# Performance work log

Hardware: AMD Instinct MI355X
Metric: run time of the kernel (lower is better)

The kernel has to match this reference:

```python
import math
import jax, jax.numpy as jnp
import numpy as np

B, N, T, C, H = 16, 307, 24, 128, 8
D = C // H
FACTOR = 5
S = min(FACTOR * int(np.ceil(np.log(T))), T)   # sample_k (U_part) = 20
U = S                                          # n_top u = 20


def _pos_emb(t_len, c):
    pos = jnp.arange(t_len, dtype=jnp.float32)[:, None]
    div = jnp.exp(jnp.arange(0, c, 2, dtype=jnp.float32) * (-math.log(10000.0) / c))
    pe = jnp.zeros((t_len, c), dtype=jnp.float32)
    pe = pe.at[:, 0::2].set(jnp.sin(pos * div))
    pe = pe.at[:, 1::2].set(jnp.cos(pos * div))
    return pe  # [T, C]


def _layernorm(x, g, b, eps=1e-5):
    m = x.mean(-1, keepdims=True)
    v = ((x - m) ** 2).mean(-1, keepdims=True)
    return (x - m) / jnp.sqrt(v + eps) * g + b


def _forward(query, time_encoder, index_sample,
             emb_minute, emb_hour, emb_weekday, emb_month, emb_year,
             Wq, Wk, Wv, Wo, bo, ff_w1, ff_b1, ff_w2, ff_b2,
             ln1_g, ln1_b, ln2_g, ln2_b):
    # DataEmbedding: x + positional + temporal (dropout = identity in eval)
    pe = _pos_emb(T, C)                                   # [T, C]
    te = (emb_minute[time_encoder[..., 0]] + emb_hour[time_encoder[..., 1]]
          + emb_weekday[time_encoder[..., 2]] + emb_month[time_encoder[..., 3]]
          + emb_year[time_encoder[..., 4]])               # [B, T, C]
    x = query + pe[None, None, :, :] + te[:, None, :, :]  # [B, N, T, C]

    # QKV projections -> [B, H, N, T, D]
    def proj(inp, W):
        return (inp @ W).reshape(B, N, T, H, D).transpose(0, 3, 1, 2, 4)
    Q, K, V = proj(x, Wq), proj(x, Wk), proj(x, Wv)

    # ProbSparse: sample S keys per query position
    K_samp = K[:, :, :, index_sample, :]                  # [B, H, N, T, S, D]
    QK_samp = jnp.einsum('bhntd,bhntsd->bhnts', Q, K_samp)
    M = QK_samp.max(-1) - QK_samp.sum(-1) / S             # [B, H, N, T]
    _, M_top = jax.lax.top_k(M, U)                        # [B, H, N, U]

    Q_red = jnp.take_along_axis(Q, M_top[..., None], axis=3)  # [B, H, N, U, D]
    scores = jnp.einsum('bhnud,bhntd->bhnut', Q_red, K) * (1.0 / math.sqrt(D))
    attn = jax.nn.softmax(scores, axis=-1)
    upd = jnp.einsum('bhnut,bhntd->bhnud', attn, V)       # [B, H, N, U, D]

    # initial context = mean over T, then scatter-update top-u query rows
    ctx = jnp.broadcast_to(V.mean(axis=3, keepdims=True), V.shape)
    ctx = ctx.at[jnp.arange(B)[:, None, None, None],
                 jnp.arange(H)[None, :, None, None],
                 jnp.arange(N)[None, None, :, None],
                 M_top].set(upd)

    ctx = ctx.transpose(0, 2, 3, 1, 4).reshape(B, N, T, C)
    att_out = ctx @ Wo + bo

    x1 = _layernorm(att_out + x, ln1_g, ln1_b)
    ff = jax.nn.relu(x1 @ ff_w1 + ff_b1) @ ff_w2 + ff_b2
    out = _layernorm(ff + x1, ln2_g, ln2_b)
    return out


def setup_inputs() -> dict:
    key = jax.random.key(0)
    ks = jax.random.split(key, 32)
    def nrm(i, shape, s=0.02):
        return jax.random.normal(ks[i], shape, dtype=jnp.float32) * s
    inp = {
        'value': jax.random.normal(ks[0], (B, N, T, C), dtype=jnp.float32),
        'key_in': jax.random.normal(ks[1], (B, N, T, C), dtype=jnp.float32),
        'query': jax.random.normal(ks[2], (B, N, T, C), dtype=jnp.float32),
        't': 1,
        'time_encoder': jax.random.randint(ks[3], (B, T, 5), 0, 10),
        'index_sample': jax.random.randint(ks[4], (T, S), 0, T),
        'emb_minute': nrm(5, (70, C), 1.0), 'emb_hour': nrm(6, (30, C), 1.0),
        'emb_weekday': nrm(7, (10, C), 1.0), 'emb_month': nrm(8, (40, C), 1.0),
        'emb_year': nrm(9, (400, C), 1.0),
        'Wq': nrm(10, (C, C)), 'Wk': nrm(11, (C, C)), 'Wv': nrm(12, (C, C)),
        'Wo': nrm(13, (C, C)), 'bo': jnp.zeros((C,), jnp.float32),
        'ff_w1': nrm(14, (C, 4 * C)), 'ff_b1': jnp.zeros((4 * C,), jnp.float32),
        'ff_w2': nrm(15, (4 * C, C)), 'ff_b2': jnp.zeros((C,), jnp.float32),
        'ln1_g': jnp.ones((C,), jnp.float32), 'ln1_b': jnp.zeros((C,), jnp.float32),
        'ln2_g': jnp.ones((C,), jnp.float32), 'ln2_b': jnp.zeros((C,), jnp.float32),
    }
    return inp


def reference(value, key_in, query, t, time_encoder, index_sample,
              emb_minute, emb_hour, emb_weekday, emb_month, emb_year,
              Wq, Wk, Wv, Wo, bo, ff_w1, ff_b1, ff_w2, ff_b2,
              ln1_g, ln1_b, ln2_g, ln2_b):
    # value, key_in, t are accepted but unused, matching the torch module
    return _forward(query, time_encoder, index_sample,
                    emb_minute, emb_hour, emb_weekday, emb_month, emb_year,
                    Wq, Wk, Wv, Wo, bo, ff_w1, ff_b1, ff_w2, ff_b2,
                    ln1_g, ln1_b, ln2_g, ln2_b)
```

## Files before the change

kernel.cpp:

```cpp
#include <hip/hip_runtime.h>
#include <hip/hip_bf16.h>
#include <cmath>

namespace {
constexpr int B_ = 16, N_ = 307, T_ = 24, C_ = 128, H_ = 8, D_ = 16, S_ = 20, U_ = 20;
constexpr int NROW = B_ * N_ * T_;
constexpr int NX = NROW * C_;
constexpr int TEPE_N = B_ * T_ * C_;
constexpr int FF = 4 * C_;
constexpr int BM = 32;
constexpr int NBLK_MM = NROW / BM;
constexpr int BMT = 32;
constexpr int NBLK_T = NROW / BMT;
constexpr int NUNIT = B_ * H_ * N_;
}

typedef __attribute__((ext_vector_type(8))) short short8;
typedef __attribute__((ext_vector_type(4))) short short4_;
typedef __attribute__((ext_vector_type(4))) float f32x4;

__device__ inline short f2bf(float v) {
    union { float f; unsigned u; } a; a.f = v;
    unsigned r = a.u + 0x7fff + ((a.u >> 16) & 1);
    return (short)(r >> 16);
}
__device__ inline float bf2f(short s) {
    return __bfloat162float(*(const __hip_bfloat16*)&s);
}

__global__ void k_tepe(const int* __restrict__ te,
                       const float* __restrict__ e_min, const float* __restrict__ e_hr,
                       const float* __restrict__ e_wd, const float* __restrict__ e_mo,
                       const float* __restrict__ e_yr, float* __restrict__ tepe,
                       const int* __restrict__ idxs, unsigned char* __restrict__ cntg) {
    int i = blockIdx.x * blockDim.x + threadIdx.x;
    if (i < TEPE_N) {
        int c = i & (C_ - 1);
        int bt = i >> 7;
        int t = bt % T_;
        const int* enc = te + bt * 5;
        float v = e_min[enc[0] * C_ + c] + e_hr[enc[1] * C_ + c] + e_wd[enc[2] * C_ + c]
                + e_mo[enc[3] * C_ + c] + e_yr[enc[4] * C_ + c];
        float ang = (float)t * expf(-(float)(c & ~1) * (9.210340371976184f / 128.0f));
        v += (c & 1) ? cosf(ang) : sinf(ang);
        tepe[i] = v;
    }
    if (blockIdx.x == 0) {
        __shared__ int scnt[T_ * 32];
        for (int j = threadIdx.x; j < T_ * 32; j += 256) scnt[j] = 0;
        __syncthreads();
        for (int j = threadIdx.x; j < T_ * S_; j += 256) {
            int t = j / S_;
            atomicAdd(&scnt[t * 32 + idxs[j]], 1);
        }
        __syncthreads();
        for (int j = threadIdx.x; j < 192; j += 256) {
            unsigned v = (unsigned)scnt[4 * j] | ((unsigned)scnt[4 * j + 1] << 8)
                       | ((unsigned)scnt[4 * j + 2] << 16) | ((unsigned)scnt[4 * j + 3] << 24);
            ((unsigned*)cntg)[j] = v;
        }
    }
}

__global__ void k_wcvt_qkv(const float* __restrict__ Wq, const float* __restrict__ Wk,
                           const float* __restrict__ Wv, short* __restrict__ wqkvf) {
    int i = blockIdx.x * 256 + threadIdx.x;
    int tile = i >> 9, l = (i >> 3) & 63, e = i & 7;
    int c_tile = tile >> 2, ks = tile & 3;
    int c_all = c_tile * 16 + (l & 15);
    int k = ks * 32 + (l >> 4) * 8 + e;
    int m = c_all >> 7, c = c_all & (C_ - 1);
    const float* W = (m == 0) ? Wq : (m == 1) ? Wk : Wv;
    wqkvf[i] = f2bf(W[k * C_ + c]);
}

__global__ void k_wcvt2(const float* __restrict__ w1, const float* __restrict__ w2,
                        const float* __restrict__ Wo,
                        short* __restrict__ w1f, short* __restrict__ w2f,
                        short* __restrict__ wof) {
    int i = blockIdx.x * 256 + threadIdx.x;
    if (i < C_ * FF) {
        int tile = i >> 9, l = (i >> 3) & 63, e = i & 7;
        int jtile = tile >> 2, ks = tile & 3;
        int j = jtile * 16 + (l & 15);
        int k = ks * 32 + (l >> 4) * 8 + e;
        w1f[i] = f2bf(w1[k * FF + j]);
    } else if (i < 2 * C_ * FF) {
        int i2 = i - C_ * FF;
        int tile = i2 >> 9, l = (i2 >> 3) & 63, e = i2 & 7;
        int c_tile = tile >> 4, ks = tile & 15;
        int c = c_tile * 16 + (l & 15);
        int j = ks * 32 + (l >> 4) * 8 + e;
        w2f[i2] = f2bf(w2[j * C_ + c]);
    } else {
        int i3 = i - 2 * C_ * FF;
        int tile = i3 >> 9, l = (i3 >> 3) & 63, e = i3 & 7;
        int c_tile = tile >> 2, ks = tile & 3;
        int c = c_tile * 16 + (l & 15);
        int k = ks * 32 + (l >> 4) * 8 + e;
        wof[i3] = f2bf(Wo[k * C_ + c]);
    }
}

__global__ __launch_bounds__(256) void k_qkv_mfma(
    const float* __restrict__ query, const float* __restrict__ tepe,
    const short* __restrict__ wqkvf,
    short* __restrict__ Q, short* __restrict__ K, short* __restrict__ V) {
    __shared__ __align__(16) short xs[BM * C_];
    int tid = threadIdx.x;
    int r0 = blockIdx.x * BM;
    {
        int row = tid >> 3;
        int cb = (tid & 7) * 16;
        int gr = r0 + row;
        int t = gr % T_;
        int b = gr / (N_ * T_);
        const float* qsrc = query + (size_t)gr * C_ + cb;
        const float* tsrc = tepe + (size_t)(b * T_ + t) * C_ + cb;
        int swz0 = (row & 7) << 3;
#pragma unroll
        for (int i = 0; i < 4; i++) {
            float4 q4 = *(const float4*)(qsrc + 4 * i);
            float4 t4 = *(const float4*)(tsrc + 4 * i);
            short4_ sv;
            sv.x = f2bf(q4.x + t4.x); sv.y = f2bf(q4.y + t4.y);
            sv.z = f2bf(q4.z + t4.z); sv.w = f2bf(q4.w + t4.w);
            *(short4_*)&xs[(row * C_ + cb + 4 * i) ^ swz0] = sv;
        }
    }
    __syncthreads();
    int w = tid >> 6, l = tid & 63;
    int lr = l & 15, lk = l >> 4;
    int swz = (lr & 7) << 3;
    short8 bx[2][4];
#pragma unroll
    for (int rt = 0; rt < 2; rt++)
#pragma unroll
        for (int ks = 0; ks < 4; ks++)
            bx[rt][ks] = *(const short8*)&xs[((rt * 16 + lr) * C_ + ks * 32 + lk * 8) ^ swz];
    size_t base[2];
#pragma unroll
    for (int rt = 0; rt < 2; rt++) {
        int gr = r0 + rt * 16 + lr;
        int t = gr % T_;
        int n = (gr / T_) % N_;
        int b = gr / (N_ * T_);
        base[rt] = ((size_t)b * H_ * N_ + n) * (T_ * D_) + t * D_;
    }
#pragma unroll
    for (int jt = 0; jt < 6; jt++) {
        int ctile = w * 6 + jt;
        const short* ap = wqkvf + (size_t)ctile * 2048 + l * 8;
        short8 acur[4];
#pragma unroll
        for (int ks = 0; ks < 4; ks++) acur[ks] = *(const short8*)(ap + ks * 512);
        f32x4 acc[2] = {{0.f, 0.f, 0.f, 0.f}, {0.f, 0.f, 0.f, 0.f}};
#pragma unroll
        for (int ks = 0; ks < 4; ks++) {
#pragma unroll
            for (int rt = 0; rt < 2; rt++)
                acc[rt] = __builtin_amdgcn_mfma_f32_16x16x32_bf16(acur[ks], bx[rt][ks], acc[rt], 0, 0, 0);
        }
        int c0 = ctile * 16 + lk * 4;
        int m = c0 >> 7;
        int c = c0 & (C_ - 1);
        int h = c >> 4, d = c & 15;
        short* dst = (m == 0) ? Q : (m == 1) ? K : V;
#pragma unroll
        for (int rt = 0; rt < 2; rt++) {
            short4_ sv;
            sv.x = f2bf(acc[rt][0]); sv.y = f2bf(acc[rt][1]);
            sv.z = f2bf(acc[rt][2]); sv.w = f2bf(acc[rt][3]);
            *(short4_*)&dst[base[rt] + (size_t)h * (N_ * T_ * D_) + d] = sv;
        }
    }
}

__global__ __launch_bounds__(256) void k_attn(
    const short* __restrict__ Q, const short* __restrict__ K, const short* __restrict__ V,
    const unsigned char* __restrict__ cntg, short* __restrict__ ctx) {
    __shared__ __align__(16) short Qbf[4][32 * 24], Kbf[4][32 * 24];
    __shared__ __align__(16) short Vt[4][16 * 40];
    __shared__ __align__(16) short Pbf[4][32 * 40];
    __shared__ unsigned char cntS[T_ * 32];
    __shared__ float Mv[4][T_];
    __shared__ int keepS[4][T_];
    __shared__ float meanVs[4][D_];
    int tid = threadIdx.x;
    int wid = tid >> 6, l = tid & 63;
    int e = blockIdx.x * 4 + wid;
    const short* qb = Q + (size_t)e * (T_ * D_);
    const short* kb = K + (size_t)e * (T_ * D_);
    const short* vb = V + (size_t)e * (T_ * D_);
    if (l < 48) {
        int t = l >> 1, hf = l & 1;
        *(short8*)&Qbf[wid][t * 24 + hf * 8] = *(const short8*)(qb + t * 16 + hf * 8);
        *(short8*)&Kbf[wid][t * 24 + hf * 8] = *(const short8*)(kb + t * 16 + hf * 8);
    }
    for (int i = l; i < 96; i += 64) {
        int t = i >> 2, c4 = i & 3;
        short4_ v = *(const short4_*)(vb + t * 16 + c4 * 4);
        Vt[wid][(c4 * 4 + 0) * 40 + t] = v.x;
        Vt[wid][(c4 * 4 + 1) * 40 + t] = v.y;
        Vt[wid][(c4 * 4 + 2) * 40 + t] = v.z;
        Vt[wid][(c4 * 4 + 3) * 40 + t] = v.w;
    }
    for (int i = l; i < 128; i += 64) {
        int d = i >> 3, c = 24 + (i & 7);
        Vt[wid][d * 40 + c] = 0;
    }
    if (tid < 192) ((int*)cntS)[tid] = ((const int*)cntg)[tid];
    __syncthreads();
    if (l >= 48) {
        int d = l - 48;
        float s = 0.f;
        for (int t = 0; t < T_; t++) s += bf2f(Vt[wid][d * 40 + t]);
        meanVs[wid][d] = s * (1.0f / T_);
    }
    int lr = l & 15, lk = l >> 4;
    short8 zz = {};
    short8 kf0 = zz, kf1 = zz, qf0 = zz, qf1 = zz;
    if (lk < 2) {
        kf0 = *(const short8*)&Kbf[wid][lr * 24 + lk * 8];
        kf1 = *(const short8*)&Kbf[wid][(16 + lr) * 24 + lk * 8];
        qf0 = *(const short8*)&Qbf[wid][lr * 24 + lk * 8];
        qf1 = *(const short8*)&Qbf[wid][(16 + lr) * 24 + lk * 8];
    }
    f32x4 zf = {0.f, 0.f, 0.f, 0.f};
    f32x4 s00 = __builtin_amdgcn_mfma_f32_16x16x32_bf16(kf0, qf0, zf, 0, 0, 0);
    f32x4 s01 = __builtin_amdgcn_mfma_f32_16x16x32_bf16(kf1, qf0, zf, 0, 0, 0);
    f32x4 s10 = __builtin_amdgcn_mfma_f32_16x16x32_bf16(kf0, qf1, zf, 0, 0, 0);
    f32x4 s11 = __builtin_amdgcn_mfma_f32_16x16x32_bf16(kf1, qf1, zf, 0, 0, 0);
#pragma unroll
    for (int rt = 0; rt < 2; rt++) {
        int t = rt * 16 + lr;
        int tt = (t < T_) ? t : 0;
        f32x4 c0 = rt ? s10 : s00;
        f32x4 c1 = rt ? s11 : s01;
        float mx = -1e30f, sm = 0.f;
#pragma unroll
        for (int i = 0; i < 4; i++) {
            int cA = cntS[tt * 32 + lk * 4 + i];
            if (cA) { mx = fmaxf(mx, c0[i]); sm += (float)cA * c0[i]; }
        }
        if (lk < 2) {
#pragma unroll
            for (int i = 0; i < 4; i++) {
                int cB = cntS[tt * 32 + 16 + lk * 4 + i];
                if (cB) { mx = fmaxf(mx, c1[i]); sm += (float)cB * c1[i]; }
            }
        }
        mx = fmaxf(mx, __shfl_xor(mx, 16));
        mx = fmaxf(mx, __shfl_xor(mx, 32));
        sm += __shfl_xor(sm, 16);
        sm += __shfl_xor(sm, 32);
        if (lk == 0 && t < T_) Mv[wid][t] = mx - sm * (1.0f / S_);
    }
    __syncthreads();
    if (l < T_) {
        float mt = Mv[wid][l];
        int cnt2 = 0;
        for (int t2 = 0; t2 < T_; t2++) {
            float m2 = Mv[wid][t2];
            cnt2 += (m2 > mt) || (m2 == mt && t2 < l);
        }
        keepS[wid][l] = (cnt2 < U_) ? 1 : 0;
    }
#pragma unroll
    for (int rt = 0; rt < 2; rt++) {
        f32x4 c0 = rt ? s10 : s00;
        f32x4 c1 = rt ? s11 : s01;
        float lm = fmaxf(fmaxf(c0[0], c0[1]), fmaxf(c0[2], c0[3]));
        if (lk < 2) lm = fmaxf(lm, fmaxf(fmaxf(c1[0], c1[1]), fmaxf(c1[2], c1[3])));
        lm = fmaxf(lm, __shfl_xor(lm, 16));
        lm = fmaxf(lm, __shfl_xor(lm, 32));
        float e0[4], e1[4];
        float ls = 0.f;
#pragma unroll
        for (int i = 0; i < 4; i++) { e0[i] = __expf(0.25f * (c0[i] - lm)); ls += e0[i]; }
#pragma unroll
        for (int i = 0; i < 4; i++) { e1[i] = (lk < 2) ? __expf(0.25f * (c1[i] - lm)) : 0.f; ls += e1[i]; }
        ls += __shfl_xor(ls, 16);
        ls += __shfl_xor(ls, 32);
        float inv = 1.0f / ls;
        short4_ w0, w1;
        w0.x = f2bf(e0[0] * inv); w0.y = f2bf(e0[1] * inv);
        w0.z = f2bf(e0[2] * inv); w0.w = f2bf(e0[3] * inv);
        w1.x = f2bf(e1[0] * inv); w1.y = f2bf(e1[1] * inv);
        w1.z = f2bf(e1[2] * inv); w1.w = f2bf(e1[3] * inv);
        int trow = rt * 16 + lr;
        *(short4_*)&Pbf[wid][trow * 40 + lk * 4] = w0;
        *(short4_*)&Pbf[wid][trow * 40 + 16 + lk * 4] = w1;
    }
    __syncthreads();
    short8 vf = *(const short8*)&Vt[wid][lr * 40 + lk * 8];
    short8 pf0 = *(const short8*)&Pbf[wid][lr * 40 + lk * 8];
    short8 pf1 = *(const short8*)&Pbf[wid][(16 + lr) * 40 + lk * 8];
    f32x4 u0 = __builtin_amdgcn_mfma_f32_16x16x32_bf16(vf, pf0, zf, 0, 0, 0);
    f32x4 u1 = __builtin_amdgcn_mfma_f32_16x16x32_bf16(vf, pf1, zf, 0, 0, 0);
    int b = e / (H_ * N_);
    int h = (e / N_) % H_;
    int n = e % N_;
    float4 mv4 = *(const float4*)&meanVs[wid][lk * 4];
#pragma unroll
    for (int rt = 0; rt < 2; rt++) {
        int t = rt * 16 + lr;
        if (t < T_) {
            f32x4 u = rt ? u1 : u0;
            float4 o;
            if (keepS[wid][t]) { o.x = u[0]; o.y = u[1]; o.z = u[2]; o.w = u[3]; }
            else o = mv4;
            short4_ sv;
            sv.x = f2bf(o.x); sv.y = f2bf(o.y); sv.z = f2bf(o.z); sv.w = f2bf(o.w);
            *(short4_*)&ctx[((size_t)(b * N_ + n) * T_ + t) * C_ + h * D_ + lk * 4] = sv;
        }
    }
}

__global__ __launch_bounds__(256, 4) void k_tail(
    const short* __restrict__ ctx, const short* __restrict__ wof, const float* __restrict__ bo,
    const float* __restrict__ query, const float* __restrict__ tepe,
    const float* __restrict__ g1, const float* __restrict__ b1,
    const short* __restrict__ w1f, const float* __restrict__ b1f,
    const short* __restrict__ w2f, const float* __restrict__ b2f,
    const float* __restrict__ g2, const float* __restrict__ b2ln,
    float* __restrict__ out) {
    __shared__ __align__(16) char smem[25088];
    float (*xf)[132] = (float(*)[132])smem;
    short* hbf = (short*)smem;
    float (*yf)[132] = (float(*)[132])smem;
    short* cbf = (short*)(smem + 16896);
    short* x1bf = (short*)(smem + 16896);
    int tid = threadIdx.x;
    int r0 = blockIdx.x * BMT;
    {
        int row = tid >> 3;
        int cb = (tid & 7) * 16;
        int gr = r0 + row;
        int t = gr % T_;
        int b = gr / (N_ * T_);
        const short* csrc = ctx + (size_t)gr * C_ + cb;
        const float* qsrc = query + (size_t)gr * C_ + cb;
        const float* tsrc = tepe + (size_t)(b * T_ + t) * C_ + cb;
        int swz0 = (row & 7) << 3;
        *(short8*)&cbf[(row * C_ + cb) ^ swz0] = *(const short8*)csrc;
        *(short8*)&cbf[(row * C_ + cb + 8) ^ swz0] = *(const short8*)(csrc + 8);
#pragma unroll
        for (int i = 0; i < 4; i++) {
            float4 q4 = *(const float4*)(qsrc + 4 * i);
            float4 t4 = *(const float4*)(tsrc + 4 * i);
            float4 xr;
            xr.x = q4.x + t4.x; xr.y = q4.y + t4.y;
            xr.z = q4.z + t4.z; xr.w = q4.w + t4.w;
            *(float4*)&xf[row][cb + 4 * i] = xr;
        }
    }
    __syncthreads();
    int w = tid >> 6, l = tid & 63;
    int lr = l & 15, lk = l >> 4;
    int swz = (lr & 7) << 3;
    {
#pragma unroll
        for (int ct = 0; ct < 2; ct++) {
            int c_tile = w * 2 + ct;
            const short* ap = wof + (size_t)c_tile * 2048 + l * 8;
            short8 acur[4];
#pragma unroll
            for (int ks = 0; ks < 4; ks++) acur[ks] = *(const short8*)(ap + ks * 512);
            f32x4 acc[2] = {{0.f, 0.f, 0.f, 0.f}, {0.f, 0.f, 0.f, 0.f}};
#pragma unroll
            for (int ks = 0; ks < 4; ks++) {
#pragma unroll
                for (int rt = 0; rt < 2; rt++) {
                    short8 bc = *(const short8*)&cbf[((rt * 16 + lr) * C_ + ks * 32 + lk * 8) ^ swz];
                    acc[rt] = __builtin_amdgcn_mfma_f32_16x16x32_bf16(acur[ks], bc, acc[rt], 0, 0, 0);
                }
            }
            int cc = c_tile * 16 + lk * 4;
            float4 bias = *(const float4*)(bo + cc);
#pragma unroll
            for (int rt = 0; rt < 2; rt++) {
                int rr = rt * 16 + lr;
                float4 res = *(const float4*)&xf[rr][cc];
                float4 o;
                o.x = acc[rt][0] + bias.x + res.x;
                o.y = acc[rt][1] + bias.y + res.y;
                o.z = acc[rt][2] + bias.z + res.z;
                o.w = acc[rt][3] + bias.w + res.w;
                *(float4*)&xf[rr][cc] = o;
            }
        }
    }
    __syncthreads();
    {
        int r = tid >> 3;
        int q = tid & 7;
        int cb = q * 16;
        float vals[16];
        float s = 0.f;
#pragma unroll
        for (int i = 0; i < 16; i++) { vals[i] = xf[r][cb + i]; s += vals[i]; }
        s += __shfl_xor(s, 1, 8);
        s += __shfl_xor(s, 2, 8);
        s += __shfl_xor(s, 4, 8);
        float mean = s * (1.f / C_);
        float vv = 0.f;
#pragma unroll
        for (int i = 0; i < 16; i++) { float d = vals[i] - mean; vv += d * d; }
        vv += __shfl_xor(vv, 1, 8);
        vv += __shfl_xor(vv, 2, 8);
        vv += __shfl_xor(vv, 4, 8);
        float rstd = rsqrtf(vv * (1.f / C_) + 1e-5f);
        short8 o0, o1;
#pragma unroll
        for (int i = 0; i < 8; i++) {
            o0[i] = f2bf((vals[i] - mean) * rstd * g1[cb + i] + b1[cb + i]);
            o1[i] = f2bf((vals[8 + i] - mean) * rstd * g1[cb + 8 + i] + b1[cb + 8 + i]);
        }
        int swz0 = (r & 7) << 3;
        *(short8*)&x1bf[(r * C_ + cb) ^ swz0] = o0;
        *(short8*)&x1bf[(r * C_ + cb + 8) ^ swz0] = o1;
    }
    __syncthreads();
    f32x4 acc2[2][2] = {{{0.f, 0.f, 0.f, 0.f}, {0.f, 0.f, 0.f, 0.f}},
                        {{0.f, 0.f, 0.f, 0.f}, {0.f, 0.f, 0.f, 0.f}}};
    for (int p = 0; p < 2; p++) {
        {
            short8 bx[2][4];
#pragma unroll
            for (int rt = 0; rt < 2; rt++)
#pragma unroll
                for (int ks = 0; ks < 4; ks++)
                    bx[rt][ks] = *(const short8*)&x1bf[((rt * 16 + lr) * C_ + ks * 32 + lk * 8) ^ swz];
#pragma unroll
            for (int jt = 0; jt < 4; jt++) {
                int jtile = p * 16 + w * 4 + jt;
                const short* ap = w1f + (size_t)jtile * 2048 + l * 8;
                short8 acur[4];
#pragma unroll
                for (int ks = 0; ks < 4; ks++) acur[ks] = *(const short8*)(ap + ks * 512);
                f32x4 acc[2] = {{0.f, 0.f, 0.f, 0.f}, {0.f, 0.f, 0.f, 0.f}};
#pragma unroll
                for (int ks = 0; ks < 4; ks++) {
#pragma unroll
                    for (int rt = 0; rt < 2; rt++)
                        acc[rt] = __builtin_amdgcn_mfma_f32_16x16x32_bf16(acur[ks], bx[rt][ks], acc[rt], 0, 0, 0);
                }
                int j0g = jtile * 16 + lk * 4;
                int j0l = (w * 4 + jt) * 16 + lk * 4;
                float4 bias = *(const float4*)(b1f + j0g);
#pragma unroll
                for (int rt = 0; rt < 2; rt++) {
                    int rr = rt * 16 + lr;
                    short4_ hv;
                    hv.x = f2bf(fmaxf(acc[rt][0] + bias.x, 0.f));
                    hv.y = f2bf(fmaxf(acc[rt][1] + bias.y, 0.f));
                    hv.z = f2bf(fmaxf(acc[rt][2] + bias.z, 0.f));
                    hv.w = f2bf(fmaxf(acc[rt][3] + bias.w, 0.f));
                    *(short4_*)&hbf[(rr * 256 + j0l) ^ swz] = hv;
                }
            }
        }
        __syncthreads();
#pragma unroll 2
        for (int ks = 0; ks < 8; ks++) {
#pragma unroll
            for (int ct = 0; ct < 2; ct++) {
                short8 aw = *(const short8*)(w2f + ((size_t)((w * 2 + ct) * 16 + p * 8 + ks)) * 512 + l * 8);
#pragma unroll
                for (int rt = 0; rt < 2; rt++) {
                    short8 hx = *(const short8*)&hbf[((rt * 16 + lr) * 256 + ks * 32 + lk * 8) ^ swz];
                    acc2[ct][rt] = __builtin_amdgcn_mfma_f32_16x16x32_bf16(aw, hx, acc2[ct][rt], 0, 0, 0);
                }
            }
        }
        __syncthreads();
    }
    {
#pragma unroll
        for (int ct = 0; ct < 2; ct++) {
            int cc = (w * 2 + ct) * 16 + lk * 4;
            float4 bias2 = *(const float4*)(b2f + cc);
#pragma unroll
            for (int rt = 0; rt < 2; rt++) {
                int rr = rt * 16 + lr;
                short4_ rb = *(const short4_*)&x1bf[(rr * C_ + cc) ^ swz];
                float4 o;
                o.x = acc2[ct][rt][0] + bias2.x + bf2f(rb.x);
                o.y = acc2[ct][rt][1] + bias2.y + bf2f(rb.y);
                o.z = acc2[ct][rt][2] + bias2.z + bf2f(rb.z);
                o.w = acc2[ct][rt][3] + bias2.w + bf2f(rb.w);
                *(float4*)&yf[rr][cc] = o;
            }
        }
    }
    __syncthreads();
    {
        int r = tid >> 3;
        int q = tid & 7;
        int cb = q * 16;
        float vals[16];
        float s = 0.f;
#pragma unroll
        for (int i = 0; i < 16; i++) { vals[i] = yf[r][cb + i]; s += vals[i]; }
        s += __shfl_xor(s, 1, 8);
        s += __shfl_xor(s, 2, 8);
        s += __shfl_xor(s, 4, 8);
        float mean = s * (1.f / C_);
        float vv = 0.f;
#pragma unroll
        for (int i = 0; i < 16; i++) { float d = vals[i] - mean; vv += d * d; }
        vv += __shfl_xor(vv, 1, 8);
        vv += __shfl_xor(vv, 2, 8);
        vv += __shfl_xor(vv, 4, 8);
        float rstd = rsqrtf(vv * (1.f / C_) + 1e-5f);
        float* op = out + (size_t)(r0 + r) * C_ + cb;
#pragma unroll
        for (int i4 = 0; i4 < 4; i4++) {
            float4 gv = *(const float4*)(g2 + cb + 4 * i4);
            float4 bv = *(const float4*)(b2ln + cb + 4 * i4);
            float4 ov;
            ov.x = (vals[4 * i4 + 0] - mean) * rstd * gv.x + bv.x;
            ov.y = (vals[4 * i4 + 1] - mean) * rstd * gv.y + bv.y;
            ov.z = (vals[4 * i4 + 2] - mean) * rstd * gv.z + bv.z;
            ov.w = (vals[4 * i4 + 3] - mean) * rstd * gv.w + bv.w;
            *(float4*)(op + 4 * i4) = ov;
        }
    }
}

extern "C" void kernel_launch(void* const* d_in, const int* in_sizes, int n_in,
                              void* d_out, int out_size, void* d_ws, size_t ws_size,
                              hipStream_t stream) {
    const float* query = (const float*)d_in[2];
    const int* time_enc = (const int*)d_in[4];
    const int* index_sample = (const int*)d_in[5];
    const float* e_min = (const float*)d_in[6];
    const float* e_hr  = (const float*)d_in[7];
    const float* e_wd  = (const float*)d_in[8];
    const float* e_mo  = (const float*)d_in[9];
    const float* e_yr  = (const float*)d_in[10];
    const float* Wq = (const float*)d_in[11];
    const float* Wk = (const float*)d_in[12];
    const float* Wv = (const float*)d_in[13];
    const float* Wo = (const float*)d_in[14];
    const float* bo = (const float*)d_in[15];
    const float* ffw1 = (const float*)d_in[16];
    const float* ffb1 = (const float*)d_in[17];
    const float* ffw2 = (const float*)d_in[18];
    const float* ffb2 = (const float*)d_in[19];
    const float* ln1g = (const float*)d_in[20];
    const float* ln1b = (const float*)d_in[21];
    const float* ln2g = (const float*)d_in[22];
    const float* ln2b = (const float*)d_in[23];

    float* ws = (float*)d_ws;
    float* tepe = ws;
    float* region1 = ws + TEPE_N;
    float* region2 = region1 + NX;
    float* region3 = region2 + NX;
    float* region4 = region3 + NX;

    short* Qb = (short*)region1;
    short* Kb = (short*)region2;
    short* Vb = (short*)region3;
    short* ctxb = (short*)region4;
    short* wqkvf = (short*)region4 + NX;
    unsigned char* cntg = (unsigned char*)((short*)region4 + NX + 49152);
    short* w1f = (short*)region2;
    short* w2f = w1f + C_ * FF;
    short* wof = w2f + C_ * FF;

    k_tepe<<<dim3(TEPE_N / 256), dim3(256), 0, stream>>>(
        time_enc, e_min, e_hr, e_wd, e_mo, e_yr, tepe, index_sample, cntg);
    k_wcvt_qkv<<<dim3(384 * C_ / 256), dim3(256), 0, stream>>>(Wq, Wk, Wv, wqkvf);
    k_qkv_mfma<<<dim3(NBLK_MM), dim3(256), 0, stream>>>(
        query, tepe, wqkvf, Qb, Kb, Vb);
    k_attn<<<dim3(NUNIT / 4), dim3(256), 0, stream>>>(
        Qb, Kb, Vb, cntg, ctxb);
    k_wcvt2<<<dim3((2 * C_ * FF + C_ * C_) / 256), dim3(256), 0, stream>>>(
        ffw1, ffw2, Wo, w1f, w2f, wof);
    k_tail<<<dim3(NBLK_T), dim3(256), 0, stream>>>(
        ctxb, wof, bo, query, tepe, ln1g, ln1b,
        w1f, ffb1, w2f, ffb2, ln2g, ln2b, (float*)d_out);
}
```

Before: 168.8 us.

## Fuse QKV projection and ProbSparse attention into one per-(b,n) kernel

Merges the QKV MFMA projection kernel and the attention kernel into a single kernel with one block per (batch, node). The Q, K and V tiles for all eight heads are written straight into shared memory instead of going to global memory and being read back, and the input x is built in registers directly from global loads. This removes the global round trip of the Q/K/V intermediates and one kernel launch. In exchange the 24-row time dimension is padded to 32 rows, which wastes some MFMA work, and shared-memory use per block rises, which may lower occupancy.

Result: slower. 203.8 us (+20.7%).

```diff
diff --git a/kernel.cpp b/kernel.cpp
--- a/kernel.cpp
+++ b/kernel.cpp
@@ -8,11 +8,9 @@
 constexpr int NX = NROW * C_;
 constexpr int TEPE_N = B_ * T_ * C_;
 constexpr int FF = 4 * C_;
-constexpr int BM = 32;
-constexpr int NBLK_MM = NROW / BM;
 constexpr int BMT = 32;
 constexpr int NBLK_T = NROW / BMT;
-constexpr int NUNIT = B_ * H_ * N_;
+constexpr int NBN = B_ * N_;
 }
 
 typedef __attribute__((ext_vector_type(8))) short short8;
@@ -102,50 +100,45 @@
     }
 }
 
-__global__ __launch_bounds__(256) void k_qkv_mfma(
+__global__ __launch_bounds__(256, 4) void k_qkv_attn(
     const float* __restrict__ query, const float* __restrict__ tepe,
-    const short* __restrict__ wqkvf,
-    short* __restrict__ Q, short* __restrict__ K, short* __restrict__ V) {
-    __shared__ __align__(16) short xs[BM * C_];
+    const short* __restrict__ wqkvf, const unsigned char* __restrict__ cntg,
+    short* __restrict__ ctx) {
+    __shared__ __align__(16) short Qbf[H_][32 * 24], Kbf[H_][32 * 24];
+    __shared__ __align__(16) short Vt[H_][16 * 40];
+    __shared__ __align__(16) short Pbf[4][32 * 40];
+    __shared__ unsigned char cntS[T_ * 32];
+    __shared__ float Mv[H_][T_];
+    __shared__ int keepS[H_][T_];
+    __shared__ float meanVs[H_][D_];
     int tid = threadIdx.x;
-    int r0 = blockIdx.x * BM;
-    {
-        int row = tid >> 3;
-        int cb = (tid & 7) * 16;
-        int gr = r0 + row;
-        int t = gr % T_;
-        int b = gr / (N_ * T_);
-        const float* qsrc = query + (size_t)gr * C_ + cb;
-        const float* tsrc = tepe + (size_t)(b * T_ + t) * C_ + cb;
-        int swz0 = (row & 7) << 3;
-#pragma unroll
-        for (int i = 0; i < 4; i++) {
-            float4 q4 = *(const float4*)(qsrc + 4 * i);
-            float4 t4 = *(const float4*)(tsrc + 4 * i);
-            short4_ sv;
-            sv.x = f2bf(q4.x + t4.x); sv.y = f2bf(q4.y + t4.y);
-            sv.z = f2bf(q4.z + t4.z); sv.w = f2bf(q4.w + t4.w);
-            *(short4_*)&xs[(row * C_ + cb + 4 * i) ^ swz0] = sv;
-        }
-    }
-    __syncthreads();
     int w = tid >> 6, l = tid & 63;
     int lr = l & 15, lk = l >> 4;
-    int swz = (lr & 7) << 3;
+    int bn = blockIdx.x;
+    int b = bn / N_;
+    size_t gr0 = (size_t)bn * T_;
+    if (tid < 192) ((int*)cntS)[tid] = ((const int*)cntg)[tid];
     short8 bx[2][4];
 #pragma unroll
-    for (int rt = 0; rt < 2; rt++)
-#pragma unroll
-        for (int ks = 0; ks < 4; ks++)
-            bx[rt][ks] = *(const short8*)&xs[((rt * 16 + lr) * C_ + ks * 32 + lk * 8) ^ swz];
-    size_t base[2];
-#pragma unroll
     for (int rt = 0; rt < 2; rt++) {
-        int gr = r0 + rt * 16 + lr;
-        int t = gr % T_;
-        int n = (gr / T_) % N_;
-        int b = gr / (N_ * T_);
-        base[rt] = ((size_t)b * H_ * N_ + n) * (T_ * D_) + t * D_;
+        int row = rt * 16 + lr;
+        int t = (row < T_) ? row : (T_ - 1);
+        const float* qsrc = query + (gr0 + t) * C_;
+        const float* tsrc = tepe + (size_t)(b * T_ + t) * C_;
+#pragma unroll
+        for (int ks = 0; ks < 4; ks++) {
+            int cb = ks * 32 + lk * 8;
+            float4 qa = *(const float4*)(qsrc + cb);
+            float4 qb4 = *(const float4*)(qsrc + cb + 4);
+            float4 ta = *(const float4*)(tsrc + cb);
+            float4 tb = *(const float4*)(tsrc + cb + 4);
+            short8 sv;
+            sv[0] = f2bf(qa.x + ta.x); sv[1] = f2bf(qa.y + ta.y);
+            sv[2] = f2bf(qa.z + ta.z); sv[3] = f2bf(qa.w + ta.w);
+            sv[4] = f2bf(qb4.x + tb.x); sv[5] = f2bf(qb4.y + tb.y);
+            sv[6] = f2bf(qb4.z + tb.z); sv[7] = f2bf(qb4.w + tb.w);
+            bx[rt][ks] = sv;
+        }
     }
 #pragma unroll
     for (int jt = 0; jt < 6; jt++) {
@@ -165,154 +158,129 @@
         int m = c0 >> 7;
         int c = c0 & (C_ - 1);
         int h = c >> 4, d = c & 15;
-        short* dst = (m == 0) ? Q : (m == 1) ? K : V;
 #pragma unroll
         for (int rt = 0; rt < 2; rt++) {
-            short4_ sv;
-            sv.x = f2bf(acc[rt][0]); sv.y = f2bf(acc[rt][1]);
-            sv.z = f2bf(acc[rt][2]); sv.w = f2bf(acc[rt][3]);
-            *(short4_*)&dst[base[rt] + (size_t)h * (N_ * T_ * D_) + d] = sv;
-        }
-    }
-}
-
-__global__ __launch_bounds__(256) void k_attn(
-    const short* __restrict__ Q, const short* __restrict__ K, const short* __restrict__ V,
-    const unsigned char* __restrict__ cntg, short* __restrict__ ctx) {
-    __shared__ __align__(16) short Qbf[4][32 * 24], Kbf[4][32 * 24];
-    __shared__ __align__(16) short Vt[4][16 * 40];
-    __shared__ __align__(16) short Pbf[4][32 * 40];
-    __shared__ unsigned char cntS[T_ * 32];
-    __shared__ float Mv[4][T_];
-    __shared__ int keepS[4][T_];
-    __shared__ float meanVs[4][D_];
-    int tid = threadIdx.x;
-    int wid = tid >> 6, l = tid & 63;
-    int e = blockIdx.x * 4 + wid;
-    const short* qb = Q + (size_t)e * (T_ * D_);
-    const short* kb = K + (size_t)e * (T_ * D_);
-    const short* vb = V + (size_t)e * (T_ * D_);
-    if (l < 48) {
-        int t = l >> 1, hf = l & 1;
-        *(short8*)&Qbf[wid][t * 24 + hf * 8] = *(const short8*)(qb + t * 16 + hf * 8);
-        *(short8*)&Kbf[wid][t * 24 + hf * 8] = *(const short8*)(kb + t * 16 + hf * 8);
-    }
-    for (int i = l; i < 96; i += 64) {
-        int t = i >> 2, c4 = i & 3;
-        short4_ v = *(const short4_*)(vb + t * 16 + c4 * 4);
-        Vt[wid][(c4 * 4 + 0) * 40 + t] = v.x;
-        Vt[wid][(c4 * 4 + 1) * 40 + t] = v.y;
-        Vt[wid][(c4 * 4 + 2) * 40 + t] = v.z;
-        Vt[wid][(c4 * 4 + 3) * 40 + t] = v.w;
-    }
-    for (int i = l; i < 128; i += 64) {
-        int d = i >> 3, c = 24 + (i & 7);
-        Vt[wid][d * 40 + c] = 0;
-    }
-    if (tid < 192) ((int*)cntS)[tid] = ((const int*)cntg)[tid];
+            int t = rt * 16 + lr;
+            if (m == 0) {
+                short4_ sv;
+                sv.x = f2bf(acc[rt][0]); sv.y = f2bf(acc[rt][1]);
+                sv.z = f2bf(acc[rt][2]); sv.w = f2bf(acc[rt][3]);
+                *(short4_*)&Qbf[h][t * 24 + d] = sv;
+            } else if (m == 1) {
+                short4_ sv;
+                sv.x = f2bf(acc[rt][0]); sv.y = f2bf(acc[rt][1]);
+                sv.z = f2bf(acc[rt][2]); sv.w = f2bf(acc[rt][3]);
+                *(short4_*)&Kbf[h][t * 24 + d] = sv;
+            } else {
+                Vt[h][(d + 0) * 40 + t] = f2bf(acc[rt][0]);
+                Vt[h][(d + 1) * 40 + t] = f2bf(acc[rt][1]);
+                Vt[h][(d + 2) * 40 + t] = f2bf(acc[rt][2]);
+                Vt[h][(d + 3) * 40 + t] = f2bf(acc[rt][3]);
+            }
+        }
+    }
     __syncthreads();
-    if (l >= 48) {
-        int d = l - 48;
-        float s = 0.f;
-        for (int t = 0; t < T_; t++) s += bf2f(Vt[wid][d * 40 + t]);
-        meanVs[wid][d] = s * (1.0f / T_);
-    }
-    int lr = l & 15, lk = l >> 4;
-    short8 zz = {};
-    short8 kf0 = zz, kf1 = zz, qf0 = zz, qf1 = zz;
-    if (lk < 2) {
-        kf0 = *(const short8*)&Kbf[wid][lr * 24 + lk * 8];
-        kf1 = *(const short8*)&Kbf[wid][(16 + lr) * 24 + lk * 8];
-        qf0 = *(const short8*)&Qbf[wid][lr * 24 + lk * 8];
-        qf1 = *(const short8*)&Qbf[wid][(16 + lr) * 24 + lk * 8];
-    }
-    f32x4 zf = {0.f, 0.f, 0.f, 0.f};
-    f32x4 s00 = __builtin_amdgcn_mfma_f32_16x16x32_bf16(kf0, qf0, zf, 0, 0, 0);
-    f32x4 s01 = __builtin_amdgcn_mfma_f32_16x16x32_bf16(kf1, qf0, zf, 0, 0, 0);
-    f32x4 s10 = __builtin_amdgcn_mfma_f32_16x16x32_bf16(kf0, qf1, zf, 0, 0, 0);
-    f32x4 s11 = __builtin_amdgcn_mfma_f32_16x16x32_bf16(kf1, qf1, zf, 0, 0, 0);
-#pragma unroll
-    for (int rt = 0; rt < 2; rt++) {
-        int t = rt * 16 + lr;
-        int tt = (t < T_) ? t : 0;
-        f32x4 c0 = rt ? s10 : s00;
-        f32x4 c1 = rt ? s11 : s01;
-        float mx = -1e30f, sm = 0.f;
-#pragma unroll
-        for (int i = 0; i < 4; i++) {
-            int cA = cntS[tt * 32 + lk * 4 + i];
-            if (cA) { mx = fmaxf(mx, c0[i]); sm += (float)cA * c0[i]; }
-        }
+    for (int hh = 0; hh < 2; hh++) {
+        int h = w * 2 + hh;
+        if (l >= 48) {
+            int d = l - 48;
+            float s = 0.f;
+            for (int t = 0; t < T_; t++) s += bf2f(Vt[h][d * 40 + t]);
+            meanVs[h][d] = s * (1.0f / T_);
+        }
+        short8 zz = {};
+        short8 kf0 = zz, kf1 = zz, qf0 = zz, qf1 = zz;
         if (lk < 2) {
+            kf0 = *(const short8*)&Kbf[h][lr * 24 + lk * 8];
+            kf1 = *(const short8*)&Kbf[h][(16 + lr) * 24 + lk * 8];
+            qf0 = *(const short8*)&Qbf[h][lr * 24 + lk * 8];
+            qf1 = *(const short8*)&Qbf[h][(16 + lr) * 24 + lk * 8];
+        }
+        f32x4 zf = {0.f, 0.f, 0.f, 0.f};
+        f32x4 s00 = __builtin_amdgcn_mfma_f32_16x16x32_bf16(kf0, qf0, zf, 0, 0, 0);
+        f32x4 s01 = __builtin_amdgcn_mfma_f32_16x16x32_bf16(kf1, qf0, zf, 0, 0, 0);
+        f32x4 s10 = __builtin_amdgcn_mfma_f32_16x16x32_bf16(kf0, qf1, zf, 0, 0, 0);
+        f32x4 s11 = __builtin_amdgcn_mfma_f32_16x16x32_bf16(kf1, qf1, zf, 0, 0, 0);
+#pragma unroll
+        for (int rt = 0; rt < 2; rt++) {
+            int t = rt * 16 + lr;
+            int tt = (t < T_) ? t : 0;
+            f32x4 c0 = rt ? s10 : s00;
+            f32x4 c1 = rt ? s11 : s01;
+            float mx = -1e30f, sm = 0.f;
 #pragma unroll
             for (int i = 0; i < 4; i++) {
-                int cB = cntS[tt * 32 + 16 + lk * 4 + i];
-                if (cB) { mx = fmaxf(mx, c1[i]); sm += (float)cB * c1[i]; }
-            }
-        }
-        mx = fmaxf(mx, __shfl_xor(mx, 16));
-        mx = fmaxf(mx, __shfl_xor(mx, 32));
-        sm += __shfl_xor(sm, 16);
-        sm += __shfl_xor(sm, 32);
-        if (lk == 0 && t < T_) Mv[wid][t] = mx - sm * (1.0f / S_);
-    }
-    __syncthreads();
-    if (l < T_) {
-        float mt = Mv[wid][l];
-        int cnt2 = 0;
-        for (int t2 = 0; t2 < T_; t2++) {
-            float m2 = Mv[wid][t2];
-            cnt2 += (m2 > mt) || (m2 == mt && t2 < l);
-        }
-        keepS[wid][l] = (cnt2 < U_) ? 1 : 0;
-    }
-#pragma unroll
-    for (int rt = 0; rt < 2; rt++) {
-        f32x4 c0 = rt ? s10 : s00;
-        f32x4 c1 = rt ? s11 : s01;
-        float lm = fmaxf(fmaxf(c0[0], c0[1]), fmaxf(c0[2], c0[3]));
-        if (lk < 2) lm = fmaxf(lm, fmaxf(fmaxf(c1[0], c1[1]), fmaxf(c1[2], c1[3])));
-        lm = fmaxf(lm, __shfl_xor(lm, 16));
-        lm = fmaxf(lm, __shfl_xor(lm, 32));
-        float e0[4], e1[4];
-        float ls = 0.f;
-#pragma unroll
-        for (int i = 0; i < 4; i++) { e0[i] = __expf(0.25f * (c0[i] - lm)); ls += e0[i]; }
-#pragma unroll
-        for (int i = 0; i < 4; i++) { e1[i] = (lk < 2) ? __expf(0.25f * (c1[i] - lm)) : 0.f; ls += e1[i]; }
-        ls += __shfl_xor(ls, 16);
-        ls += __shfl_xor(ls, 32);
-        float inv = 1.0f / ls;
-        short4_ w0, w1;
-        w0.x = f2bf(e0[0] * inv); w0.y = f2bf(e0[1] * inv);
-        w0.z = f2bf(e0[2] * inv); w0.w = f2bf(e0[3] * inv);
-        w1.x = f2bf(e1[0] * inv); w1.y = f2bf(e1[1] * inv);
-        w1.z = f2bf(e1[2] * inv); w1.w = f2bf(e1[3] * inv);
-        int trow = rt * 16 + lr;
-        *(short4_*)&Pbf[wid][trow * 40 + lk * 4] = w0;
-        *(short4_*)&Pbf[wid][trow * 40 + 16 + lk * 4] = w1;
-    }
-    __syncthreads();
-    short8 vf = *(const short8*)&Vt[wid][lr * 40 + lk * 8];
-    short8 pf0 = *(const short8*)&Pbf[wid][lr * 40 + lk * 8];
-    short8 pf1 = *(const short8*)&Pbf[wid][(16 + lr) * 40 + lk * 8];
-    f32x4 u0 = __builtin_amdgcn_mfma_f32_16x16x32_bf16(vf, pf0, zf, 0, 0, 0);
-    f32x4 u1 = __builtin_amdgcn_mfma_f32_16x16x32_bf16(vf, pf1, zf, 0, 0, 0);
-    int b = e / (H_ * N_);
-    int h = (e / N_) % H_;
-    int n = e % N_;
-    float4 mv4 = *(const float4*)&meanVs[wid][lk * 4];
-#pragma unroll
-    for (int rt = 0; rt < 2; rt++) {
-        int t = rt * 16 + lr;
-        if (t < T_) {
-            f32x4 u = rt ? u1 : u0;
-            float4 o;
-            if (keepS[wid][t]) { o.x = u[0]; o.y = u[1]; o.z = u[2]; o.w = u[3]; }
-            else o = mv4;
-            short4_ sv;
-            sv.x = f2bf(o.x); sv.y = f2bf(o.y); sv.z = f2bf(o.z); sv.w = f2bf(o.w);
-            *(short4_*)&ctx[((size_t)(b * N_ + n) * T_ + t) * C_ + h * D_ + lk * 4] = sv;
+                int cA = cntS[tt * 32 + lk * 4 + i];
+                if (cA) { mx = fmaxf(mx, c0[i]); sm += (float)cA * c0[i]; }
+            }
+            if (lk < 2) {
+#pragma unroll
+                for (int i = 0; i < 4; i++) {
+                    int cB = cntS[tt * 32 + 16 + lk * 4 + i];
+                    if (cB) { mx = fmaxf(mx, c1[i]); sm += (float)cB * c1[i]; }
+                }
+            }
+            mx = fmaxf(mx, __shfl_xor(mx, 16));
+            mx = fmaxf(mx, __shfl_xor(mx, 32));
+            sm += __shfl_xor(sm, 16);
+            sm += __shfl_xor(sm, 32);
+            if (lk == 0 && t < T_) Mv[h][t] = mx - sm * (1.0f / S_);
+        }
+        __syncthreads();
+        if (l < T_) {
+            float mt = Mv[h][l];
+            int cnt2 = 0;
+            for (int t2 = 0; t2 < T_; t2++) {
+                float m2 = Mv[h][t2];
+                cnt2 += (m2 > mt) || (m2 == mt && t2 < l);
+            }
+            keepS[h][l] = (cnt2 < U_) ? 1 : 0;
+        }
+#pragma unroll
+        for (int rt = 0; rt < 2; rt++) {
+            f32x4 c0 = rt ? s10 : s00;
+            f32x4 c1 = rt ? s11 : s01;
+            float lm = fmaxf(fmaxf(c0[0], c0[1]), fmaxf(c0[2], c0[3]));
+            if (lk < 2) lm = fmaxf(lm, fmaxf(fmaxf(c1[0], c1[1]), fmaxf(c1[2], c1[3])));
+            lm = fmaxf(lm, __shfl_xor(lm, 16));
+            lm = fmaxf(lm, __shfl_xor(lm, 32));
+            float e0[4], e1[4];
+            float ls = 0.f;
+#pragma unroll
+            for (int i = 0; i < 4; i++) { e0[i] = __expf(0.25f * (c0[i] - lm)); ls += e0[i]; }
+#pragma unroll
+            for (int i = 0; i < 4; i++) { e1[i] = (lk < 2) ? __expf(0.25f * (c1[i] - lm)) : 0.f; ls += e1[i]; }
+            ls += __shfl_xor(ls, 16);
+            ls += __shfl_xor(ls, 32);
+            float inv = 1.0f / ls;
+            short4_ w0, w1;
+            w0.x = f2bf(e0[0] * inv); w0.y = f2bf(e0[1] * inv);
+            w0.z = f2bf(e0[2] * inv); w0.w = f2bf(e0[3] * inv);
+            w1.x = f2bf(e1[0] * inv); w1.y = f2bf(e1[1] * inv);
+            w1.z = f2bf(e1[2] * inv); w1.w = f2bf(e1[3] * inv);
+            int trow = rt * 16 + lr;
+            *(short4_*)&Pbf[w][trow * 40 + lk * 4] = w0;
+            *(short4_*)&Pbf[w][trow * 40 + 16 + lk * 4] = w1;
+        }
+        __syncthreads();
+        short8 vf = *(const short8*)&Vt[h][lr * 40 + lk * 8];
+        short8 pf0 = *(const short8*)&Pbf[w][lr * 40 + lk * 8];
+        short8 pf1 = *(const short8*)&Pbf[w][(16 + lr) * 40 + lk * 8];
+        f32x4 u0 = __builtin_amdgcn_mfma_f32_16x16x32_bf16(vf, pf0, zf, 0, 0, 0);
+        f32x4 u1 = __builtin_amdgcn_mfma_f32_16x16x32_bf16(vf, pf1, zf, 0, 0, 0);
+        float4 mv4 = *(const float4*)&meanVs[h][lk * 4];
+#pragma unroll
+        for (int rt = 0; rt < 2; rt++) {
+            int t = rt * 16 + lr;
+            if (t < T_) {
+                f32x4 u = rt ? u1 : u0;
+                float4 o;
+                if (keepS[h][t]) { o.x = u[0]; o.y = u[1]; o.z = u[2]; o.w = u[3]; }
+                else o = mv4;
+                short4_ sv;
+                sv.x = f2bf(o.x); sv.y = f2bf(o.y); sv.z = f2bf(o.z); sv.w = f2bf(o.w);
+                *(short4_*)&ctx[((size_t)bn * T_ + t) * C_ + h * D_ + lk * 4] = sv;
+            }
         }
     }
 }
@@ -556,14 +524,9 @@
 
     float* ws = (float*)d_ws;
     float* tepe = ws;
-    float* region1 = ws + TEPE_N;
-    float* region2 = region1 + NX;
-    float* region3 = region2 + NX;
-    float* region4 = region3 + NX;
-
-    short* Qb = (short*)region1;
-    short* Kb = (short*)region2;
-    short* Vb = (short*)region3;
+    float* region2 = ws + TEPE_N + NX;
+    float* region4 = region2 + 2 * NX;
+
     short* ctxb = (short*)region4;
     short* wqkvf = (short*)region4 + NX;
     unsigned char* cntg = (unsigned char*)((short*)region4 + NX + 49152);
@@ -574,12 +537,10 @@
     k_tepe<<<dim3(TEPE_N / 256), dim3(256), 0, stream>>>(
         time_enc, e_min, e_hr, e_wd, e_mo, e_yr, tepe, index_sample, cntg);
     k_wcvt_qkv<<<dim3(384 * C_ / 256), dim3(256), 0, stream>>>(Wq, Wk, Wv, wqkvf);
-    k_qkv_mfma<<<dim3(NBLK_MM), dim3(256), 0, stream>>>(
-        query, tepe, wqkvf, Qb, Kb, Vb);
-    k_attn<<<dim3(NUNIT / 4), dim3(256), 0, stream>>>(
-        Qb, Kb, Vb, cntg, ctxb);
     k_wcvt2<<<dim3((2 * C_ * FF + C_ * C_) / 256), dim3(256), 0, stream>>>(
         ffw1, ffw2, Wo, w1f, w2f, wof);
+    k_qkv_attn<<<dim3(NBN), dim3(256), 0, stream>>>(
+        query, tepe, wqkvf, cntg, ctxb);
     k_tail<<<dim3(NBLK_T), dim3(256), 0, stream>>>(
         ctxb, wof, bo, query, tepe, ln1g, ln1b,
         w1f, ffb1, w2f, ffb2, ln2g, ln2b, (float*)d_out);
```
